# Kernel tuning notes

Measured on AMD Instinct MI355X. Metric: run time of the kernel, lower is better.

The kernel has to match this reference:

```python
import jax, jax.numpy as jnp
import numpy as np

DIM = 128
RES = 64
H_SP, W_SP = 64, 4   # idx == 0: H_sp = resolution, W_sp = split_size
NUM_HEADS = 4
HEAD_DIM = DIM // NUM_HEADS
SCALE = HEAD_DIM ** -0.5


def img2windows(img, H_sp, W_sp):
    # img: (B, C, H, W) -> (B*nHw*nWw, H_sp*W_sp, C)
    B, C, H, W = img.shape
    x = img.reshape(B, C, H // H_sp, H_sp, W // W_sp, W_sp)
    x = jnp.transpose(x, (0, 2, 4, 3, 5, 1))
    return x.reshape(-1, H_sp * W_sp, C)


def windows2img(wins, H_sp, W_sp, H, W):
    C = wins.shape[-1]
    B = wins.shape[0] // ((H // H_sp) * (W // W_sp))
    x = wins.reshape(B, H // H_sp, W // W_sp, H_sp, W_sp, C)
    x = jnp.transpose(x, (0, 5, 1, 3, 2, 4))
    return x.reshape(B, C, H, W)


def im2cswin(x, H_sp, W_sp, num_heads):
    # (B, C, H, W) -> (B', num_heads, L, head_dim)
    C = x.shape[1]
    w = img2windows(x, H_sp, W_sp)                       # (B', L, C)
    w = w.reshape(-1, H_sp * W_sp, num_heads, C // num_heads)
    return jnp.transpose(w, (0, 2, 1, 3))


def conv1x1(x, w, b):
    # x: (B, C, H, W), w: (O, C), b: (O,)
    return jnp.einsum('bchw,oc->bohw', x, w) + b[None, :, None, None]


def depthwise5x5(x, w, b):
    # x: (B, C, H, W), w: (C, 1, 5, 5) depthwise, pad=2
    y = jax.lax.conv_general_dilated(
        x, w, window_strides=(1, 1), padding=((2, 2), (2, 2)),
        feature_group_count=x.shape[1],
        dimension_numbers=('NCHW', 'OIHW', 'NCHW'))
    return y + b[None, :, None, None]


def setup_inputs() -> dict:
    key = jax.random.key(0)
    ks = jax.random.split(key, 8)
    B = 16
    x = jax.random.normal(ks[0], (B, DIM, RES, RES), dtype=jnp.float32)
    n_windows = B * (RES // H_SP) * (RES // W_SP)
    L = H_SP * W_SP
    attn_input = jax.random.normal(ks[1], (n_windows, NUM_HEADS, L, L), dtype=jnp.float32)
    s = 0.02
    wq = jax.random.normal(ks[2], (DIM, DIM), dtype=jnp.float32) * s
    bq = jnp.zeros((DIM,), dtype=jnp.float32)
    wv = jax.random.normal(ks[3], (DIM, DIM), dtype=jnp.float32) * s
    bv = jnp.zeros((DIM,), dtype=jnp.float32)
    w_lepe = jax.random.normal(ks[4], (DIM, 1, 5, 5), dtype=jnp.float32) * s
    b_lepe = jnp.zeros((DIM,), dtype=jnp.float32)
    temperature = jnp.ones((NUM_HEADS, 1, 1), dtype=jnp.float32)
    return {"x": x, "attn_input": attn_input, "wq": wq, "bq": bq,
            "wv": wv, "bv": bv, "w_lepe": w_lepe, "b_lepe": b_lepe,
            "temperature": temperature}


def reference(x, attn_input, wq, bq, wv, bv, w_lepe, b_lepe, temperature):
    B, C, H, W = x.shape
    v_map = conv1x1(x, wv, bv)
    lepe = depthwise5x5(v_map, w_lepe, b_lepe)           # (B, C, H, W)
    # shift_size == 0: no roll
    q_map = conv1x1(x, wq, bq)
    q = im2cswin(q_map + lepe, H_SP, W_SP, NUM_HEADS) * SCALE  # (B', nh, L, d)
    k = im2cswin(x + lepe, H_SP, W_SP, NUM_HEADS)
    v = im2cswin(v_map, H_SP, W_SP, NUM_HEADS)
    scores = jnp.einsum('whqd,whkd->whqk', q, k)         # (B', nh, L, L)
    attn = jax.nn.softmax(scores, axis=-1) + temperature[None] * attn_input
    out = jnp.einsum('whqk,whkd->whqd', attn, v)         # (B', nh, L, d)
    out = jnp.transpose(out, (0, 2, 1, 3)).reshape(-1, H_SP * W_SP, C)
    out = windows2img(out, H_SP, W_SP, H, W)             # (B, C, H, W)
    return (out + lepe, attn)
```

## Files before the change

### kernel.cpp

```cpp
#include <hip/hip_runtime.h>

typedef __attribute__((ext_vector_type(4)))  float fx4;
typedef __attribute__((ext_vector_type(16))) float fx16;
typedef __attribute__((ext_vector_type(8)))  short bf8;

#define SCALE 0.17677669529663687f

__device__ __forceinline__ unsigned short f2bf(float f) {
  unsigned int u = __builtin_bit_cast(unsigned int, f);
  unsigned int r = (u + 0x7fffu + ((u >> 16) & 1u)) >> 16;
  return (unsigned short)r;
}
__device__ __forceinline__ float bf2f(unsigned short u) {
  unsigned int v = ((unsigned int)u) << 16;
  return __builtin_bit_cast(float, v);
}

__global__ __launch_bounds__(256) void k0_xT(const float* __restrict__ x,
                                             unsigned short* __restrict__ xT) {
  int h = blockIdx.x, b = blockIdx.y, t = threadIdx.x;
  __shared__ unsigned short tile[128 * 68];
  const float* xrow = x + ((size_t)b * 128 * 4096) + h * 64;
#pragma unroll
  for (int i = 0; i < 8; ++i) {
    int slot = t + i * 256;
    int c = slot >> 4, wq = slot & 15;
    float4 v = *reinterpret_cast<const float4*>(xrow + (size_t)c * 4096 + wq * 4);
    unsigned short* p = &tile[c * 68 + wq * 4];
    p[0] = f2bf(v.x); p[1] = f2bf(v.y); p[2] = f2bf(v.z); p[3] = f2bf(v.w);
  }
  __syncthreads();
  int w = t >> 2, cc = t & 3;
  unsigned short tmp[32];
#pragma unroll
  for (int j = 0; j < 32; ++j) tmp[j] = tile[(cc * 32 + j) * 68 + w];
  unsigned short* dst = xT + ((size_t)(b * 4096 + h * 64 + w)) * 128 + cc * 32;
#pragma unroll
  for (int q = 0; q < 4; ++q)
    *reinterpret_cast<bf8*>(dst + q * 8) = *reinterpret_cast<bf8*>(tmp + q * 8);
}

__global__ __launch_bounds__(256) void k1_conv(const unsigned short* __restrict__ xT,
    const float* __restrict__ wq, const float* __restrict__ bq,
    const float* __restrict__ wv, const float* __restrict__ bv,
    unsigned short* __restrict__ qT, unsigned short* __restrict__ vT) {
  int pt = blockIdx.x, b = blockIdx.y, qv = blockIdx.z;
  const float* W = qv ? wv : wq;
  const float* bias = qv ? bv : bq;
  unsigned short* out = qv ? vT : qT;
  int t = threadIdx.x, lane = t & 63, wave = t >> 6;
  int wm = wave >> 1, wn = wave & 1;
  int l31 = lane & 31, g2 = lane >> 5;
  fx16 acc[2][2] = {};
  const unsigned short* Abase = xT + ((size_t)b * 4096 + pt * 128) * 128;
#pragma unroll
  for (int ks = 0; ks < 8; ++ks) {
    int kbase = ks * 16 + g2 * 8;
    bf8 a[2], bb[2];
#pragma unroll
    for (int mi = 0; mi < 2; ++mi) {
      int pix = (wm * 2 + mi) * 32 + l31;
      a[mi] = *reinterpret_cast<const bf8*>(Abase + (size_t)pix * 128 + kbase);
    }
#pragma unroll
    for (int ni = 0; ni < 2; ++ni) {
      int oc = (wn * 2 + ni) * 32 + l31;
      const float* wp = W + oc * 128 + kbase;
      float4 w0 = *reinterpret_cast<const float4*>(wp);
      float4 w1 = *reinterpret_cast<const float4*>(wp + 4);
      bf8 r;
      r[0]=(short)f2bf(w0.x); r[1]=(short)f2bf(w0.y); r[2]=(short)f2bf(w0.z); r[3]=(short)f2bf(w0.w);
      r[4]=(short)f2bf(w1.x); r[5]=(short)f2bf(w1.y); r[6]=(short)f2bf(w1.z); r[7]=(short)f2bf(w1.w);
      bb[ni] = r;
    }
#pragma unroll
    for (int mi = 0; mi < 2; ++mi)
#pragma unroll
      for (int ni = 0; ni < 2; ++ni)
        acc[mi][ni] = __builtin_amdgcn_mfma_f32_32x32x16_bf16(a[mi], bb[ni], acc[mi][ni], 0, 0, 0);
  }
#pragma unroll
  for (int ni = 0; ni < 2; ++ni) {
    int oc = (wn * 2 + ni) * 32 + l31;
    float bsv = bias[oc];
#pragma unroll
    for (int mi = 0; mi < 2; ++mi) {
#pragma unroll
      for (int r = 0; r < 16; ++r) {
        int row = (r & 3) + 8 * (r >> 2) + 4 * g2;
        int pix = pt * 128 + (wm * 2 + mi) * 32 + row;
        out[((size_t)b * 4096 + pix) * 128 + oc] = f2bf(acc[mi][ni][r] + bsv);
      }
    }
  }
}

__global__ __launch_bounds__(256) void k2_lepe(const unsigned short* __restrict__ vT,
    const float* __restrict__ wl5, const float* __restrict__ bl,
    float* __restrict__ lepe) {
  int strip = blockIdx.x, hd = blockIdx.y, b = blockIdx.z;
  int t = threadIdx.x;
  __shared__ unsigned short tile[12 * 64 * 34];
  int h0 = strip * 8;
#pragma unroll
  for (int i = 0; i < 12; ++i) {
    int slot = t + i * 256;
    int r = slot >> 8;
    int rem = slot & 255;
    int w = rem >> 2, cc = rem & 3;
    int h = h0 - 2 + r;
    unsigned short vv[8];
    if (h >= 0 && h < 64) {
      *reinterpret_cast<bf8*>(vv) = *reinterpret_cast<const bf8*>(
          vT + ((size_t)b * 4096 + h * 64 + w) * 128 + hd * 32 + cc * 8);
    } else {
#pragma unroll
      for (int j = 0; j < 8; ++j) vv[j] = 0;
    }
    unsigned int* dst = reinterpret_cast<unsigned int*>(&tile[(r * 64 + w) * 34 + cc * 8]);
#pragma unroll
    for (int j = 0; j < 4; ++j)
      dst[j] = ((unsigned int)vv[2 * j + 1] << 16) | (unsigned int)vv[2 * j];
  }
  __syncthreads();
  int c2 = t & 15, w16 = t >> 4;
  int c = c2 * 2;
  float wt0[25], wt1[25];
#pragma unroll
  for (int i = 0; i < 25; ++i) {
    wt0[i] = wl5[(hd * 32 + c) * 25 + i];
    wt1[i] = wl5[(hd * 32 + c + 1) * 25 + i];
  }
  float b0 = bl[hd * 32 + c], b1 = bl[hd * 32 + c + 1];
  for (int hh = 0; hh < 8; ++hh) {
    for (int wi = 0; wi < 4; ++wi) {
      int w = w16 * 4 + wi;
      float a0 = b0, a1 = b1;
#pragma unroll
      for (int dy = 0; dy < 5; ++dy) {
        int rr = hh + dy;
#pragma unroll
        for (int dx = 0; dx < 5; ++dx) {
          int wx = w + dx - 2;
          if (wx < 0 || wx >= 64) continue;
          unsigned int pr = *reinterpret_cast<const unsigned int*>(&tile[(rr * 64 + wx) * 34 + c]);
          float v0 = bf2f((unsigned short)(pr & 0xffffu));
          float v1 = bf2f((unsigned short)(pr >> 16));
          a0 += v0 * wt0[dy * 5 + dx];
          a1 += v1 * wt1[dy * 5 + dx];
        }
      }
      float2 st; st.x = a0; st.y = a1;
      *reinterpret_cast<float2*>(&lepe[((size_t)b * 4096 + (h0 + hh) * 64 + w) * 128 + hd * 32 + c]) = st;
    }
  }
}

__device__ __forceinline__ bf8 frag_add(const unsigned short* xp, const float* lp, float scale) {
  bf8 xv = *reinterpret_cast<const bf8*>(xp);
  float4 l0 = *reinterpret_cast<const float4*>(lp);
  float4 l1 = *reinterpret_cast<const float4*>(lp + 4);
  bf8 r;
  r[0] = (short)f2bf((bf2f((unsigned short)xv[0]) + l0.x) * scale);
  r[1] = (short)f2bf((bf2f((unsigned short)xv[1]) + l0.y) * scale);
  r[2] = (short)f2bf((bf2f((unsigned short)xv[2]) + l0.z) * scale);
  r[3] = (short)f2bf((bf2f((unsigned short)xv[3]) + l0.w) * scale);
  r[4] = (short)f2bf((bf2f((unsigned short)xv[4]) + l1.x) * scale);
  r[5] = (short)f2bf((bf2f((unsigned short)xv[5]) + l1.y) * scale);
  r[6] = (short)f2bf((bf2f((unsigned short)xv[6]) + l1.z) * scale);
  r[7] = (short)f2bf((bf2f((unsigned short)xv[7]) + l1.w) * scale);
  return r;
}

__global__ __launch_bounds__(256, 2) void k3_attn(
    const unsigned short* __restrict__ xT, const unsigned short* __restrict__ qT,
    const unsigned short* __restrict__ vT, const float* __restrict__ lepe,
    const float* __restrict__ ai, const float* __restrict__ temp,
    float* __restrict__ attn, float* __restrict__ out_win) {
  int w = blockIdx.x;
  int hd = blockIdx.y;
  int b = w >> 4, ww = w & 15;
  int t = threadIdx.x, lane = t & 63, wave = t >> 6;
  int l15 = lane & 15, g = lane >> 4;
  __shared__ unsigned short Vt[32 * 264];

  {
    int l = t;
    int pix = (l >> 2) * 64 + ww * 4 + (l & 3);
    const unsigned short* src = vT + ((size_t)b * 4096 + pix) * 128 + hd * 32;
    unsigned short vv[32];
#pragma unroll
    for (int q = 0; q < 4; ++q)
      *reinterpret_cast<bf8*>(vv + q * 8) = *reinterpret_cast<const bf8*>(src + q * 8);
#pragma unroll
    for (int d = 0; d < 32; ++d) Vt[d * 264 + l] = vv[d];
  }
  __syncthreads();
  float tHd = temp[hd];

  bf8 kf[16];
#pragma unroll
  for (int nt = 0; nt < 16; ++nt) {
    int kpos = nt * 16 + l15;
    int pix = (kpos >> 2) * 64 + ww * 4 + (kpos & 3);
    size_t off = ((size_t)b * 4096 + pix) * 128 + hd * 32 + g * 8;
    kf[nt] = frag_add(xT + off, lepe + off, 1.0f);
  }

  const size_t aBase = ((size_t)w * 4 + hd) * 256 * 256;
  const float* aiB = ai + aBase;
  float* atB = attn + aBase;
  float* owB = out_win + ((size_t)w * 4 + hd) * 256 * 32;

  for (int pass = 0; pass < 4; ++pass) {
    int qbase = (pass * 4 + wave) * 16;
    bf8 qf;
    {
      int qrow = qbase + l15;
      int pix = (qrow >> 2) * 64 + ww * 4 + (qrow & 3);
      size_t off = ((size_t)b * 4096 + pix) * 128 + hd * 32 + g * 8;
      qf = frag_add(qT + off, lepe + off, SCALE);
    }
    fx4 acc[16];
#pragma unroll
    for (int nt = 0; nt < 16; ++nt) { acc[nt][0]=0.f; acc[nt][1]=0.f; acc[nt][2]=0.f; acc[nt][3]=0.f; }
#pragma unroll
    for (int nt = 0; nt < 16; ++nt)
      acc[nt] = __builtin_amdgcn_mfma_f32_16x16x32_bf16(qf, kf[nt], acc[nt], 0, 0, 0);

    float inv[4];
#pragma unroll
    for (int r = 0; r < 4; ++r) {
      float m = acc[0][r];
#pragma unroll
      for (int nt = 1; nt < 16; ++nt) m = fmaxf(m, acc[nt][r]);
      m = fmaxf(m, __shfl_xor(m, 1));
      m = fmaxf(m, __shfl_xor(m, 2));
      m = fmaxf(m, __shfl_xor(m, 4));
      m = fmaxf(m, __shfl_xor(m, 8));
      float s = 0.f;
#pragma unroll
      for (int nt = 0; nt < 16; ++nt) {
        float p = __expf(acc[nt][r] - m);
        acc[nt][r] = p;
        s += p;
      }
      s += __shfl_xor(s, 1); s += __shfl_xor(s, 2);
      s += __shfl_xor(s, 4); s += __shfl_xor(s, 8);
      inv[r] = 1.0f / s;
    }

#pragma unroll
    for (int nt = 0; nt < 16; ++nt) {
#pragma unroll
      for (int r = 0; r < 4; ++r) {
        int row = qbase + g * 4 + r;
        int col = nt * 16 + l15;
        size_t idx = (size_t)row * 256 + col;
        atB[idx] = acc[nt][r] * inv[r] + tHd * aiB[idx];
      }
    }
    asm volatile("s_waitcnt vmcnt(0)" ::: "memory");

    fx4 oacc[2];
    oacc[0][0]=0.f;oacc[0][1]=0.f;oacc[0][2]=0.f;oacc[0][3]=0.f;
    oacc[1][0]=0.f;oacc[1][1]=0.f;oacc[1][2]=0.f;oacc[1][3]=0.f;
#pragma unroll
    for (int ks = 0; ks < 8; ++ks) {
      const float* ap = atB + (size_t)(qbase + l15) * 256 + ks * 32 + g * 8;
      float4 a0 = *reinterpret_cast<const float4*>(ap);
      float4 a1 = *reinterpret_cast<const float4*>(ap + 4);
      bf8 af;
      af[0]=(short)f2bf(a0.x); af[1]=(short)f2bf(a0.y); af[2]=(short)f2bf(a0.z); af[3]=(short)f2bf(a0.w);
      af[4]=(short)f2bf(a1.x); af[5]=(short)f2bf(a1.y); af[6]=(short)f2bf(a1.z); af[7]=(short)f2bf(a1.w);
#pragma unroll
      for (int nt2 = 0; nt2 < 2; ++nt2) {
        bf8 vf = *reinterpret_cast<const bf8*>(&Vt[(nt2 * 16 + l15) * 264 + ks * 32 + g * 8]);
        oacc[nt2] = __builtin_amdgcn_mfma_f32_16x16x32_bf16(af, vf, oacc[nt2], 0, 0, 0);
      }
    }
#pragma unroll
    for (int nt2 = 0; nt2 < 2; ++nt2)
#pragma unroll
      for (int r = 0; r < 4; ++r) {
        int row = qbase + g * 4 + r;
        owB[(size_t)row * 32 + nt2 * 16 + l15] = oacc[nt2][r];
      }
  }
}

__global__ __launch_bounds__(256) void k4_out(const float* __restrict__ out_win,
    const float* __restrict__ lepe, float* __restrict__ out0) {
  int h = blockIdx.x, b = blockIdx.y, t = threadIdx.x;
  __shared__ float winb[16 * 533];
  __shared__ float lep[64 * 129];
#pragma unroll
  for (int i = 0; i < 8; ++i) {
    int slot = t + i * 256;
    int ww = slot >> 7, rem = slot & 127;
    int hdq = rem >> 5, rem2 = rem & 31;
    int wl = rem2 >> 3, dq = rem2 & 7;
    float4 v = *reinterpret_cast<const float4*>(
        out_win + (((size_t)(b * 16 + ww) * 4 + hdq) * 256 + h * 4 + wl) * 32 + dq * 4);
    float* p = &winb[ww * 533 + wl * 133 + hdq * 33 + dq * 4];
    p[0] = v.x; p[1] = v.y; p[2] = v.z; p[3] = v.w;
  }
#pragma unroll
  for (int i = 0; i < 8; ++i) {
    int slot = t + i * 256;
    int w = slot >> 5, cq = slot & 31;
    float4 v = *reinterpret_cast<const float4*>(
        lepe + ((size_t)b * 4096 + h * 64 + w) * 128 + cq * 4);
    float* p = &lep[w * 129 + cq * 4];
    p[0] = v.x; p[1] = v.y; p[2] = v.z; p[3] = v.w;
  }
  __syncthreads();
  int w = t & 63, cg = t >> 6;
#pragma unroll
  for (int ci = 0; ci < 32; ++ci) {
    int c = cg * 32 + ci;
    float val = winb[(w >> 2) * 533 + (w & 3) * 133 + (c >> 5) * 33 + (c & 31)] + lep[w * 129 + c];
    out0[((size_t)(b * 128 + c) * 64 + h) * 64 + w] = val;
  }
}

extern "C" void kernel_launch(void* const* d_in, const int* in_sizes, int n_in,
                              void* d_out, int out_size, void* d_ws, size_t ws_size,
                              hipStream_t stream) {
  const float* x    = (const float*)d_in[0];
  const float* ai   = (const float*)d_in[1];
  const float* wq   = (const float*)d_in[2];
  const float* bq   = (const float*)d_in[3];
  const float* wv   = (const float*)d_in[4];
  const float* bv   = (const float*)d_in[5];
  const float* wl5  = (const float*)d_in[6];
  const float* bl   = (const float*)d_in[7];
  const float* temp = (const float*)d_in[8];
  float* out0 = (float*)d_out;
  float* attn = out0 + 8388608;

  char* ws = (char*)d_ws;
  unsigned short* xT = (unsigned short*)(ws);
  unsigned short* qT = (unsigned short*)(ws + 16777216);
  unsigned short* vT = (unsigned short*)(ws + 33554432);
  float* lepe        = (float*)(ws + 50331648);
  float* ow          = (float*)(ws + 83886080);

  k0_xT  <<<dim3(64, 16),    256, 0, stream>>>(x, xT);
  k1_conv<<<dim3(32, 16, 2), 256, 0, stream>>>(xT, wq, bq, wv, bv, qT, vT);
  k2_lepe<<<dim3(8, 4, 16),  256, 0, stream>>>(vT, wl5, bl, lepe);
  k3_attn<<<dim3(256, 4),    256, 0, stream>>>(xT, qT, vT, lepe, ai, temp, attn, ow);
  k4_out <<<dim3(64, 16),    256, 0, stream>>>(ow, lepe, out0);
}
```

Measured before the change: 289.8 us.

## Stage softmax probabilities in LDS instead of re-reading attn from global

The score MFMA now runs with operands swapped, so each lane holds a full query row slice. The row max and sum then need only two cross-lane shuffles, and the ai reads and attn writes become float4 vectors. The normalized probabilities are converted to bf16 and written into a per-wave LDS buffer, which feeds the PV MFMA. This replaces the global readback that followed a full vmcnt wait. Occupancy is also raised to 3 blocks per SM, at the cost of extra LDS per block and tighter register limits.

```diff
diff --git a/kernel.cpp b/kernel.cpp
--- a/kernel.cpp
+++ b/kernel.cpp
@@ -3,6 +3,7 @@
 typedef __attribute__((ext_vector_type(4)))  float fx4;
 typedef __attribute__((ext_vector_type(16))) float fx16;
 typedef __attribute__((ext_vector_type(8)))  short bf8;
+typedef __attribute__((ext_vector_type(4)))  short bf4;
 
 #define SCALE 0.17677669529663687f
 
@@ -172,7 +173,7 @@
   return r;
 }
 
-__global__ __launch_bounds__(256, 2) void k3_attn(
+__global__ __launch_bounds__(256, 3) void k3_attn(
     const unsigned short* __restrict__ xT, const unsigned short* __restrict__ qT,
     const unsigned short* __restrict__ vT, const float* __restrict__ lepe,
     const float* __restrict__ ai, const float* __restrict__ temp,
@@ -183,6 +184,7 @@
   int t = threadIdx.x, lane = t & 63, wave = t >> 6;
   int l15 = lane & 15, g = lane >> 4;
   __shared__ unsigned short Vt[32 * 264];
+  __shared__ unsigned short P[4][16 * 264];
 
   {
     int l = t;
@@ -211,6 +213,7 @@
   const float* aiB = ai + aBase;
   float* atB = attn + aBase;
   float* owB = out_win + ((size_t)w * 4 + hd) * 256 * 32;
+  unsigned short* Pw = &P[wave][0];
 
   for (int pass = 0; pass < 4; ++pass) {
     int qbase = (pass * 4 + wave) * 16;
@@ -221,58 +224,54 @@
       size_t off = ((size_t)b * 4096 + pix) * 128 + hd * 32 + g * 8;
       qf = frag_add(qT + off, lepe + off, SCALE);
     }
-    fx4 acc[16];
-#pragma unroll
-    for (int nt = 0; nt < 16; ++nt) { acc[nt][0]=0.f; acc[nt][1]=0.f; acc[nt][2]=0.f; acc[nt][3]=0.f; }
+    fx4 acc[16] = {};
 #pragma unroll
     for (int nt = 0; nt < 16; ++nt)
-      acc[nt] = __builtin_amdgcn_mfma_f32_16x16x32_bf16(qf, kf[nt], acc[nt], 0, 0, 0);
-
-    float inv[4];
-#pragma unroll
-    for (int r = 0; r < 4; ++r) {
-      float m = acc[0][r];
-#pragma unroll
-      for (int nt = 1; nt < 16; ++nt) m = fmaxf(m, acc[nt][r]);
-      m = fmaxf(m, __shfl_xor(m, 1));
-      m = fmaxf(m, __shfl_xor(m, 2));
-      m = fmaxf(m, __shfl_xor(m, 4));
-      m = fmaxf(m, __shfl_xor(m, 8));
-      float s = 0.f;
-#pragma unroll
-      for (int nt = 0; nt < 16; ++nt) {
+      acc[nt] = __builtin_amdgcn_mfma_f32_16x16x32_bf16(kf[nt], qf, acc[nt], 0, 0, 0);
+
+    float m = acc[0][0];
+#pragma unroll
+    for (int nt = 0; nt < 16; ++nt) {
+#pragma unroll
+      for (int r = 0; r < 4; ++r) m = fmaxf(m, acc[nt][r]);
+    }
+    m = fmaxf(m, __shfl_xor(m, 16));
+    m = fmaxf(m, __shfl_xor(m, 32));
+    float s = 0.f;
+#pragma unroll
+    for (int nt = 0; nt < 16; ++nt) {
+#pragma unroll
+      for (int r = 0; r < 4; ++r) {
         float p = __expf(acc[nt][r] - m);
         acc[nt][r] = p;
         s += p;
       }
-      s += __shfl_xor(s, 1); s += __shfl_xor(s, 2);
-      s += __shfl_xor(s, 4); s += __shfl_xor(s, 8);
-      inv[r] = 1.0f / s;
-    }
-
+    }
+    s += __shfl_xor(s, 16);
+    s += __shfl_xor(s, 32);
+    float inv = 1.0f / s;
+
+    int qrow = qbase + l15;
 #pragma unroll
     for (int nt = 0; nt < 16; ++nt) {
-#pragma unroll
-      for (int r = 0; r < 4; ++r) {
-        int row = qbase + g * 4 + r;
-        int col = nt * 16 + l15;
-        size_t idx = (size_t)row * 256 + col;
-        atB[idx] = acc[nt][r] * inv[r] + tHd * aiB[idx];
-      }
-    }
-    asm volatile("s_waitcnt vmcnt(0)" ::: "memory");
-
-    fx4 oacc[2];
-    oacc[0][0]=0.f;oacc[0][1]=0.f;oacc[0][2]=0.f;oacc[0][3]=0.f;
-    oacc[1][0]=0.f;oacc[1][1]=0.f;oacc[1][2]=0.f;oacc[1][3]=0.f;
+      size_t idx = (size_t)qrow * 256 + nt * 16 + g * 4;
+      float4 av = *reinterpret_cast<const float4*>(aiB + idx);
+      float4 sv;
+      sv.x = acc[nt][0] * inv + tHd * av.x;
+      sv.y = acc[nt][1] * inv + tHd * av.y;
+      sv.z = acc[nt][2] * inv + tHd * av.z;
+      sv.w = acc[nt][3] * inv + tHd * av.w;
+      *reinterpret_cast<float4*>(atB + idx) = sv;
+      bf4 pb;
+      pb[0] = (short)f2bf(sv.x); pb[1] = (short)f2bf(sv.y);
+      pb[2] = (short)f2bf(sv.z); pb[3] = (short)f2bf(sv.w);
+      *reinterpret_cast<bf4*>(&Pw[l15 * 264 + nt * 16 + g * 4]) = pb;
+    }
+
+    fx4 oacc[2] = {};
 #pragma unroll
     for (int ks = 0; ks < 8; ++ks) {
-      const float* ap = atB + (size_t)(qbase + l15) * 256 + ks * 32 + g * 8;
-      float4 a0 = *reinterpret_cast<const float4*>(ap);
-      float4 a1 = *reinterpret_cast<const float4*>(ap + 4);
-      bf8 af;
-      af[0]=(short)f2bf(a0.x); af[1]=(short)f2bf(a0.y); af[2]=(short)f2bf(a0.z); af[3]=(short)f2bf(a0.w);
-      af[4]=(short)f2bf(a1.x); af[5]=(short)f2bf(a1.y); af[6]=(short)f2bf(a1.z); af[7]=(short)f2bf(a1.w);
+      bf8 af = *reinterpret_cast<const bf8*>(&Pw[l15 * 264 + ks * 32 + g * 8]);
 #pragma unroll
       for (int nt2 = 0; nt2 < 2; ++nt2) {
         bf8 vf = *reinterpret_cast<const bf8*>(&Vt[(nt2 * 16 + l15) * 264 + ks * 32 + g * 8]);
```

Measured after the change: 320.1 us. 1.1x slower.
